# Kernel optimization log

Measured on AMD Instinct MI355X. Metric: run time of the kernel, lower is better.

The kernel has to match this reference:

```python
import jax, jax.numpy as jnp
import numpy as np

N_FLUID = 16384
N_BND = 2048
SUPPORT = float(np.sqrt(16.0 / (np.pi * N_FLUID)))  # ~16 neighbors avg
NB = 8  # basis functions per axis (n = m = 8)
NM = NB * NB
LAYERS = [32, 64, 64, 2]
F_IN = 8
B_IN = 8


def _radius(queries, points, r):
    """numpy brute-force (chunked) radius search; rows = query idx, cols = point idx."""
    r2 = np.float32(r * r)
    pn = (points ** 2).sum(-1)
    qi_all, pj_all = [], []
    for s in range(0, queries.shape[0], 4096):
        q = queries[s:s + 4096]
        d2 = (q ** 2).sum(-1)[:, None] + pn[None, :] - 2.0 * (q @ points.T)
        qi, pj = np.nonzero(d2 < r2)
        qi_all.append(qi + s)
        pj_all.append(pj)
    return (np.concatenate(qi_all).astype(np.int32),
            np.concatenate(pj_all).astype(np.int32))


def setup_inputs() -> dict:
    rng = np.random.default_rng(0)
    fluid_pos = rng.random((N_FLUID, 2)).astype(np.float32)
    # boundary particles along the perimeter of the unit square
    t = np.linspace(0.0, 4.0, N_BND, endpoint=False).astype(np.float32)
    side = np.floor(t).astype(np.int64)
    frac = t - side
    bx = np.where(side == 0, frac, np.where(side == 1, 1.0, np.where(side == 2, 1.0 - frac, 0.0)))
    by = np.where(side == 0, 0.0, np.where(side == 1, frac, np.where(side == 2, 1.0, 1.0 - frac)))
    bnd_pos = np.stack([bx, by], -1).astype(np.float32)

    # fluid-fluid radius graph (centerIgnore: drop self edges)
    fi, fj = _radius(fluid_pos, fluid_pos, SUPPORT)
    keep = fi != fj
    f_tgt, f_src = fi[keep], fj[keep]
    # fluid(query) - boundary(source) radius graph
    b_tgt, b_src = _radius(fluid_pos, bnd_pos, SUPPORT)

    def conv_w(k, cin, cout):
        return (0.05 * rng.standard_normal((NM, cin, cout))).astype(np.float32)

    def lin_w(cin, cout):
        s = np.sqrt(6.0 / (cin + cout))
        return rng.uniform(-s, s, (cin, cout)).astype(np.float32)

    d = {
        'fluid_pos': jnp.asarray(fluid_pos),
        'bnd_pos': jnp.asarray(bnd_pos),
        'fluid_feat': jnp.asarray(rng.standard_normal((N_FLUID, F_IN)).astype(np.float32)),
        'bnd_feat': jnp.asarray(rng.standard_normal((N_BND, B_IN)).astype(np.float32)),
        'f_tgt': jnp.asarray(f_tgt), 'f_src': jnp.asarray(f_src),
        'b_tgt': jnp.asarray(b_tgt), 'b_src': jnp.asarray(b_src),
        # convs: c0 fluid->fluid (F_IN->32), c1 boundary->fluid (B_IN->32),
        #        c2 (96->64), c3 (64->64), c4 (64->2)
        'Wc0': jnp.asarray(conv_w(0, F_IN, 32)), 'bc0': jnp.zeros((32,), jnp.float32),
        'Wc1': jnp.asarray(conv_w(1, B_IN, 32)), 'bc1': jnp.zeros((32,), jnp.float32),
        'Wc2': jnp.asarray(conv_w(2, 96, 64)), 'bc2': jnp.zeros((64,), jnp.float32),
        'Wc3': jnp.asarray(conv_w(3, 64, 64)), 'bc3': jnp.zeros((64,), jnp.float32),
        'Wc4': jnp.asarray(conv_w(4, 64, 2)), 'bc4': jnp.zeros((2,), jnp.float32),
        # dense branch: l0 (F_IN->32), l1 (96->64), l2 (64->64), l3 (64->2)
        'Wl0': jnp.asarray(lin_w(F_IN, 32)), 'bl0': jnp.zeros((32,), jnp.float32),
        'Wl1': jnp.asarray(lin_w(96, 64)), 'bl1': jnp.zeros((64,), jnp.float32),
        'Wl2': jnp.asarray(lin_w(64, 64)), 'bl2': jnp.zeros((64,), jnp.float32),
        'Wl3': jnp.asarray(lin_w(64, 2)), 'bl3': jnp.zeros((2,), jnp.float32),
    }
    return d


def _hat(x, n):
    # linear 'hat' RBF basis on centers in [-1, 1]
    c = jnp.linspace(-1.0, 1.0, n, dtype=x.dtype)
    return jnp.maximum(0.0, 1.0 - jnp.abs(x[:, None] - c[None, :]) * ((n - 1) / 2.0))


def _polar(d):
    # polar coordinate mapping of normalized displacement d in [-1,1]^2
    r = jnp.sqrt(jnp.sum(d * d, -1) + 1e-12)
    theta = jnp.arctan2(d[:, 1], d[:, 0])
    return jnp.clip(jnp.stack([2.0 * r - 1.0, theta / jnp.pi], -1), -1.0, 1.0)


def _rbf_conv(x_src_nodes, src, tgt, disp, W, b, num_tgt):
    m = _polar(disp)                                   # [E,2]
    bx = _hat(m[:, 0], NB)                             # [E,n]
    by = _hat(m[:, 1], NB)                             # [E,m]
    basis = (bx[:, :, None] * by[:, None, :]).reshape(-1, NM)  # [E,nm]
    xs = x_src_nodes[src]                              # [E,cin]
    acc0 = jnp.zeros((xs.shape[0], W.shape[-1]), xs.dtype)

    def body(acc, wb):
        Wk, bk = wb
        return acc + bk[:, None] * (xs @ Wk), None

    msg, _ = jax.lax.scan(body, acc0, (W, basis.T))    # sum_k basis_k * (xs @ W_k)
    return jax.ops.segment_sum(msg, tgt, num_segments=num_tgt) + b


def reference(fluid_pos, bnd_pos, fluid_feat, bnd_feat, f_tgt, f_src, b_tgt, b_src,
              Wc0, bc0, Wc1, bc1, Wc2, bc2, Wc3, bc3, Wc4, bc4,
              Wl0, bl0, Wl1, bl1, Wl2, bl2, Wl3, bl3):
    N = fluid_feat.shape[0]
    fdisp = jnp.clip(-(fluid_pos[f_src] - fluid_pos[f_tgt]) / SUPPORT, -1.0, 1.0)
    bdisp = jnp.clip((bnd_pos[b_src] - fluid_pos[b_tgt]) / SUPPORT, -1.0, 1.0)

    lin = fluid_feat @ Wl0 + bl0
    fconv = _rbf_conv(fluid_feat, f_src, f_tgt, fdisp, Wc0, bc0, N)
    bconv = _rbf_conv(bnd_feat, b_src, b_tgt, bdisp, Wc1, bc1, N)
    ans = jnp.concatenate([lin, fconv, bconv], axis=-1)  # [N, 96]

    blocks = [(Wc2, bc2, Wl1, bl1, False), (Wc3, bc3, Wl2, bl2, True), (Wc4, bc4, Wl3, bl3, False)]
    for Wc, bc, Wl, bl, residual in blocks:
        a = jax.nn.relu(ans)
        c = _rbf_conv(a, f_src, f_tgt, fdisp, Wc, bc, N)
        dns = a @ Wl + bl
        ans = c + dns + ans if residual else c + dns
    return ans / 128.0
```

## Files before the change

kernel.cpp:

```cpp
#include <hip/hip_runtime.h>
#include <math.h>
#include <stdint.h>

#define NFL   16384
#define NCC   55
#define PADQ  128

struct EdgeData { int src; int ixiy; float fx; float fy; };

typedef _Float16 half8 __attribute__((ext_vector_type(8)));
typedef __attribute__((ext_vector_type(4))) float f32x4;

__device__ __forceinline__ float frelu(float x){ return x > 0.f ? x : 0.f; }
__device__ __forceinline__ unsigned short f2bf(float f){
    unsigned int u = __float_as_uint(f);
    unsigned int r = (u + 0x7FFFu + ((u >> 16) & 1u)) >> 16;
    return (unsigned short)r;
}

__device__ __forceinline__ EdgeData make_edge(const float* qpos, const float* ppos,
                                              int t, int s, float support, float sgn)
{
    float dx = sgn * (ppos[2*s]   - qpos[2*t])   / support;
    float dy = sgn * (ppos[2*s+1] - qpos[2*t+1]) / support;
    dx = fminf(1.f, fmaxf(-1.f, dx));
    dy = fminf(1.f, fmaxf(-1.f, dy));
    float r  = sqrtf(dx*dx + dy*dy + 1e-12f);
    float th = atan2f(dy, dx);
    float m0 = fminf(1.f, fmaxf(-1.f, 2.f*r - 1.f));
    float m1 = fminf(1.f, fmaxf(-1.f, th * 0.3183098861837907f));
    float u = (m0 + 1.f) * 3.5f;
    float v = (m1 + 1.f) * 3.5f;
    int ix = (int)u; if (ix > 6) ix = 6;
    int iy = (int)v; if (iy > 6) iy = 6;
    EdgeData ed;
    ed.src  = s;
    ed.ixiy = ix*8 + iy;
    ed.fx   = u - (float)ix;
    ed.fy   = v - (float)iy;
    return ed;
}

__global__ __launch_bounds__(256)
void setup_k(const float* __restrict__ fluid_pos, const float* __restrict__ bnd_pos,
             const int* __restrict__ f_tgt, const int* __restrict__ f_src, int nEf,
             const int* __restrict__ b_tgt, const int* __restrict__ b_src, int nEb,
             float support,
             EdgeData* __restrict__ edF, EdgeData* __restrict__ edB,
             int* __restrict__ cnt,
             int* __restrict__ rowptrF, int* __restrict__ rowptrB,
             int nA, int nB, int nC)
{
    int b = blockIdx.x, tid = threadIdx.x;
    if (b < nA){
        __shared__ int lc[64];
        if (tid < 64) lc[tid] = 0;
        __syncthreads();
        int e = b*256 + tid;
        if (e < nEf){
            EdgeData d = make_edge(fluid_pos, fluid_pos, f_tgt[e], f_src[e], support, -1.f);
            edF[e] = d;
            atomicAdd(&lc[d.ixiy], 1);
        }
        __syncthreads();
        if (tid < 64 && lc[tid] > 0) atomicAdd(&cnt[tid], lc[tid]);
    } else if (b < nA + nB){
        int e = (b - nA)*256 + tid;
        if (e < nEb)
            edB[e] = make_edge(fluid_pos, bnd_pos, b_tgt[e], b_src[e], support, 1.f);
    } else if (b < nA + nB + nC){
        int t = (b - nA - nB)*256 + tid;
        if (t > NFL) return;
        if (t == NFL){ rowptrF[NFL] = nEf; return; }
        int lo = 0, hi = nEf;
        while (lo < hi){ int mid = (lo + hi) >> 1; if (f_tgt[mid] < t) lo = mid + 1; else hi = mid; }
        rowptrF[t] = lo;
    } else {
        int t = (b - nA - nB - nC)*256 + tid;
        if (t > NFL) return;
        if (t == NFL){ rowptrB[NFL] = nEb; return; }
        int lo = 0, hi = nEb;
        while (lo < hi){ int mid = (lo + hi) >> 1; if (b_tgt[mid] < t) lo = mid + 1; else hi = mid; }
        rowptrB[t] = lo;
    }
}

__global__ __launch_bounds__(256)
void scan_pad_k(const int* __restrict__ cnt, int* __restrict__ cellOff,
                int* __restrict__ gcursor, int4* __restrict__ entries)
{
    __shared__ int offS[NCC+1], cntS[NCC];
    int tid = threadIdx.x;
    if (tid < 64) gcursor[tid] = 0;
    if (tid == 0){
        int s = 0;
        for (int k = 0; k < NCC; ++k){
            offS[k] = s; int c = cnt[k]; cntS[k] = c;
            s += ((c + PADQ - 1) / PADQ) * PADQ;
        }
        offS[NCC] = s;
        for (int k = 0; k <= NCC; ++k) cellOff[k] = offS[k];
    }
    __syncthreads();
    for (int k = 0; k < NCC; ++k){
        int base = offS[k] + cntS[k];
        int pads = (offS[k+1] - offS[k]) - cntS[k];
        for (int i = tid; i < pads; i += 256)
            entries[base + i] = make_int4(0, -1, 0, 0);
    }
}

__global__ void scatter_k(const EdgeData* __restrict__ ed, int nE,
                          const int* __restrict__ cellOff,
                          int* __restrict__ gcursor,
                          int4* __restrict__ entries)
{
    __shared__ int lc[64], base[64];
    int tid = threadIdx.x;
    if (tid < 64) lc[tid] = 0;
    __syncthreads();
    int e = blockIdx.x * blockDim.x + tid;
    bool ok = e < nE;
    EdgeData d; int k = 0, r = 0;
    if (ok){ d = ed[e]; k = d.ixiy; r = atomicAdd(&lc[k], 1); }
    __syncthreads();
    if (tid < 64 && lc[tid] > 0) base[tid] = atomicAdd(&gcursor[tid], lc[tid]);
    __syncthreads();
    if (ok){
        int slot = cellOff[k] + base[k] + r;
        entries[slot] = make_int4(d.src, e, __float_as_int(d.fx), __float_as_int(d.fy));
    }
}

__global__ __launch_bounds__(256)
void wprep_k(const float* __restrict__ Wc2, const float* __restrict__ Wc3,
             const float* __restrict__ Wc0,
             _Float16* __restrict__ wt2, _Float16* __restrict__ wt3,
             unsigned short* __restrict__ wb0)
{
    __shared__ _Float16 T[64][98];
    int b = blockIdx.x, tid = threadIdx.x;
    if (b < 64){
        const float* s = Wc2 + (size_t)b * 96 * 64;
        for (int i = tid; i < 96*64; i += 256){ int k = i/64, c = i - k*64; T[c][k] = (_Float16)s[i]; }
        __syncthreads();
        _Float16* d = wt2 + (size_t)b * 64 * 96;
        for (int i = tid; i < 96*64; i += 256){ int c = i/96, k = i - c*96; d[i] = T[c][k]; }
    } else if (b < 128){
        int cell = b - 64;
        const float* s = Wc3 + (size_t)cell * 64 * 64;
        for (int i = tid; i < 64*64; i += 256){ int k = i/64, c = i - k*64; T[c][k] = (_Float16)s[i]; }
        __syncthreads();
        _Float16* d = wt3 + (size_t)cell * 64 * 64;
        for (int i = tid; i < 64*64; i += 256){ int c = i/64, k = i - c*64; d[i] = T[c][k]; }
    } else {
        for (int i = tid; i < 64*8*32; i += 256) wb0[i] = f2bf(Wc0[i]);
    }
}

template<int CIN>
__global__ __launch_bounds__(256)
void conv_mfma_k(const _Float16* __restrict__ xh,
                 const int4* __restrict__ entries,
                 const int* __restrict__ cellOff,
                 const _Float16* __restrict__ wt,
                 _Float16* __restrict__ msg)
{
    constexpr int COUT = 64;
    constexpr int XROW = CIN*2 + 16;
    constexpr int C16  = CIN*2/16;

    __shared__ unsigned char XL[64 * XROW];
    __shared__ float BW[4][64];
    __shared__ int   SRC[64];
    __shared__ int   EID[64];

    int total = cellOff[NCC];
    int pb = blockIdx.x * 128;
    if (pb >= total) return;
    int tid = threadIdx.x;

    int lo_ = 0, hi_ = NCC;
    while (hi_ - lo_ > 1){ int mid = (lo_ + hi_) >> 1; if (cellOff[mid] <= pb) lo_ = mid; else hi_ = mid; }
    const int cell = lo_;
    const int kc[4] = { cell, cell+1, cell+8, cell+9 };

    const int lane = tid & 63, wv = tid >> 6;
    const int lr = lane & 15, lg = lane >> 4;
    const int cb = wv * 16;
    const _Float16* wbase = wt + (size_t)(cb + lr) * CIN + lg * 8;

    for (int ch = 0; ch < 2; ++ch){
        int p0 = pb + ch * 64;

        if (tid < 64){
            int4 en = entries[p0 + tid];
            bool ok = en.y >= 0;
            float fx = __int_as_float(en.z), fy = __int_as_float(en.w);
            BW[0][tid] = ok ? (1.f-fx)*(1.f-fy) : 0.f;
            BW[1][tid] = ok ? (1.f-fx)*fy       : 0.f;
            BW[2][tid] = ok ? fx*(1.f-fy)       : 0.f;
            BW[3][tid] = ok ? fx*fy             : 0.f;
            SRC[tid] = en.x;
            EID[tid] = en.y;
        }
        __syncthreads();
        for (int i = tid; i < 64*C16; i += 256){
            int e = i / C16, c = i - e*C16;
            const uint4* sp = (const uint4*)(xh + (size_t)SRC[e]*CIN) + c;
            *(uint4*)(&XL[e*XROW + 16*c]) = *sp;
        }
        __syncthreads();

        f32x4 acc[4][4];
#pragma unroll
        for (int cr = 0; cr < 4; ++cr)
#pragma unroll
            for (int ae = 0; ae < 4; ++ae)
                acc[cr][ae] = (f32x4)0.f;

#pragma unroll
        for (int k0 = 0; k0 < CIN; k0 += 32){
            half8 b[4], a[4];
#pragma unroll
            for (int cr = 0; cr < 4; ++cr)
                b[cr] = *(const half8*)(wbase + (size_t)kc[cr]*(COUT*CIN) + k0);
#pragma unroll
            for (int ae = 0; ae < 4; ++ae)
                a[ae] = *(const half8*)(XL + (16*ae + lr)*XROW + k0*2 + lg*16);
#pragma unroll
            for (int cr = 0; cr < 4; ++cr)
#pragma unroll
                for (int ae = 0; ae < 4; ++ae)
                    acc[cr][ae] = __builtin_amdgcn_mfma_f32_16x16x32_f16(a[ae], b[cr], acc[cr][ae], 0, 0, 0);
        }

#pragma unroll
        for (int ae = 0; ae < 4; ++ae){
#pragma unroll
            for (int r = 0; r < 4; ++r){
                int E = 16*ae + lg*4 + r;
                int eid = EID[E];
                if (eid >= 0){
                    float v = BW[0][E]*acc[0][ae][r] + BW[1][E]*acc[1][ae][r]
                            + BW[2][E]*acc[2][ae][r] + BW[3][E]*acc[3][ae][r];
                    msg[(size_t)eid*COUT + cb + lr] = (_Float16)v;
                }
            }
        }
        __syncthreads();
    }
}

template<int CIN, int COUT, int TILE_E, bool RELU>
__global__ __launch_bounds__(128)
void conv_cell_k(const float* __restrict__ x,
                 const int4* __restrict__ entries,
                 const int* __restrict__ cellOff,
                 const unsigned short* __restrict__ Wbf,
                 _Float16* __restrict__ msg)
{
    constexpr int TEP = TILE_E + 4;
    constexpr int EG  = TILE_E / 4;
    constexpr int CG  = COUT / 8;
    static_assert(EG * CG == 128, "tile/thread mismatch");
    constexpr int C4  = CIN / 4;

    __shared__ float XT[CIN][TEP];
    __shared__ unsigned short WLc[4][CIN][COUT];
    __shared__ int4 EN[TILE_E];

    int total = cellOff[NCC];
    int p0 = blockIdx.x * TILE_E;
    if (p0 >= total) return;
    int tid = threadIdx.x;

    int lo = 0, hi = NCC;
    while (hi - lo > 1){ int mid = (lo + hi) >> 1; if (cellOff[mid] <= p0) lo = mid; else hi = mid; }
    const int cell = lo;

    for (int i = tid; i < TILE_E; i += 128) EN[i] = entries[p0 + i];

    const int kc[4] = { cell, cell + 1, cell + 8, cell + 9 };
#pragma unroll
    for (int c = 0; c < 4; ++c){
        const uint4* s = (const uint4*)(Wbf + (size_t)kc[c] * (CIN * COUT));
        uint4* dlds = (uint4*)(&WLc[c][0][0]);
        for (int i = tid; i < CIN * COUT / 8; i += 128) dlds[i] = s[i];
    }
    __syncthreads();

    for (int i = tid; i < TILE_E * C4; i += 128){
        int e  = i / C4;
        int c4 = i - e * C4;
        int4 en = EN[e];
        float4 v = make_float4(0.f, 0.f, 0.f, 0.f);
        if (en.y >= 0){
            v = *(const float4*)(x + (size_t)en.x * CIN + 4 * c4);
            if (RELU){ v.x = frelu(v.x); v.y = frelu(v.y); v.z = frelu(v.z); v.w = frelu(v.w); }
        }
        XT[4*c4+0][e] = v.x;
        XT[4*c4+1][e] = v.y;
        XT[4*c4+2][e] = v.z;
        XT[4*c4+3][e] = v.w;
    }
    __syncthreads();

    const int egrp = tid % EG;
    const int cgrp = tid / EG;
    const int e0 = egrp * 4;

    float fx[4], fy[4];
    int eid[4];
#pragma unroll
    for (int j = 0; j < 4; ++j){
        int4 en = EN[e0 + j];
        fx[j] = __int_as_float(en.z);
        fy[j] = __int_as_float(en.w);
        eid[j] = en.y;
    }

    float accT[4][8];
#pragma unroll
    for (int j = 0; j < 4; ++j)
#pragma unroll
        for (int c = 0; c < 8; ++c) accT[j][c] = 0.f;

#pragma unroll
    for (int cr = 0; cr < 4; ++cr){
        float accC[4][8];
#pragma unroll
        for (int j = 0; j < 4; ++j)
#pragma unroll
            for (int c = 0; c < 8; ++c) accC[j][c] = 0.f;

#pragma unroll
        for (int ci = 0; ci < CIN; ++ci){
            float4 xv = *(const float4*)&XT[ci][e0];
            uint4 wp = *(const uint4*)&WLc[cr][ci][cgrp * 8];
            float wf0 = __uint_as_float(wp.x << 16);
            float wf1 = __uint_as_float(wp.x & 0xFFFF0000u);
            float wf2 = __uint_as_float(wp.y << 16);
            float wf3 = __uint_as_float(wp.y & 0xFFFF0000u);
            float wf4 = __uint_as_float(wp.z << 16);
            float wf5 = __uint_as_float(wp.z & 0xFFFF0000u);
            float wf6 = __uint_as_float(wp.w << 16);
            float wf7 = __uint_as_float(wp.w & 0xFFFF0000u);
            const float xe[4] = { xv.x, xv.y, xv.z, xv.w };
#pragma unroll
            for (int j = 0; j < 4; ++j){
                accC[j][0] += xe[j] * wf0;
                accC[j][1] += xe[j] * wf1;
                accC[j][2] += xe[j] * wf2;
                accC[j][3] += xe[j] * wf3;
                accC[j][4] += xe[j] * wf4;
                accC[j][5] += xe[j] * wf5;
                accC[j][6] += xe[j] * wf6;
                accC[j][7] += xe[j] * wf7;
            }
        }
#pragma unroll
        for (int j = 0; j < 4; ++j){
            float wc = (cr == 0) ? (1.f - fx[j]) * (1.f - fy[j]) :
                       (cr == 1) ? (1.f - fx[j]) * fy[j] :
                       (cr == 2) ? fx[j] * (1.f - fy[j]) :
                                   fx[j] * fy[j];
#pragma unroll
            for (int c = 0; c < 8; ++c) accT[j][c] += wc * accC[j][c];
        }
    }

#pragma unroll
    for (int j = 0; j < 4; ++j){
        if (eid[j] < 0) continue;
        half8 hv;
#pragma unroll
        for (int c = 0; c < 8; ++c) hv[c] = (_Float16)accT[j][c];
        *(half8*)(msg + (size_t)eid[j] * COUT + cgrp * 8) = hv;
    }
}

__global__ __launch_bounds__(128)
void conv2_msg_k(const _Float16* __restrict__ xh,
                 const int4* __restrict__ entries,
                 const int* __restrict__ cellOff,
                 const float* __restrict__ Wc,
                 float* __restrict__ msg2)
{
    __shared__ float WLf[4][64][2];
    int total = cellOff[NCC];
    int p0 = blockIdx.x * 128;
    if (p0 >= total) return;
    int tid = threadIdx.x;

    int lo = 0, hi = NCC;
    while (hi - lo > 1){ int mid = (lo + hi) >> 1; if (cellOff[mid] <= p0) lo = mid; else hi = mid; }
    const int cell = lo;
    const int kc[4] = { cell, cell + 1, cell + 8, cell + 9 };
#pragma unroll
    for (int c = 0; c < 4; ++c)
        ((float*)&WLf[c][0][0])[tid] = Wc[(size_t)kc[c] * 128 + tid];
    __syncthreads();

    int4 en = entries[p0 + tid];
    if (en.y < 0) return;
    float fx = __int_as_float(en.z), fy = __int_as_float(en.w);
    const _Float16* xp = xh + (size_t)en.x * 64;

    float a[4][2] = {{0.f,0.f},{0.f,0.f},{0.f,0.f},{0.f,0.f}};
#pragma unroll
    for (int ci = 0; ci < 64; ci += 8){
        half8 v = *(const half8*)(xp + ci);
#pragma unroll
        for (int j = 0; j < 8; ++j){
            float xe = (float)v[j];
#pragma unroll
            for (int cr = 0; cr < 4; ++cr){
                a[cr][0] += xe * WLf[cr][ci+j][0];
                a[cr][1] += xe * WLf[cr][ci+j][1];
            }
        }
    }
    float w0 = (1.f-fx)*(1.f-fy), w1 = (1.f-fx)*fy, w2 = fx*(1.f-fy), w3 = fx*fy;
    float m0 = w0*a[0][0] + w1*a[1][0] + w2*a[2][0] + w3*a[3][0];
    float m1 = w0*a[0][1] + w1*a[1][1] + w2*a[2][1] + w3*a[3][1];
    *(float2*)(msg2 + (size_t)en.y * 2) = make_float2(m0, m1);
}

__global__ __launch_bounds__(256)
void final_combine_k(const float* __restrict__ y2,
                     const float* __restrict__ Wl3, const float* __restrict__ bl3,
                     const float* __restrict__ bc4,
                     const float* __restrict__ msg2,
                     const int* __restrict__ rowptr,
                     float* __restrict__ out)
{
    __shared__ float WS[128];
    int tid = threadIdx.x;
    if (tid < 128) WS[tid] = Wl3[tid];
    __syncthreads();

    int t = blockIdx.x * blockDim.x + tid;
    if (t >= NFL) return;
    int eb = rowptr[t], ee = rowptr[t+1];

    float a0 = bc4[0] + bl3[0];
    float a1 = bc4[1] + bl3[1];
    const float* pr = y2 + (size_t)t * 64;
#pragma unroll 4
    for (int ci = 0; ci < 64; ci += 4){
        float4 v = *(const float4*)(pr + ci);
        float xe[4] = { frelu(v.x), frelu(v.y), frelu(v.z), frelu(v.w) };
#pragma unroll
        for (int j = 0; j < 4; ++j){
            a0 += xe[j] * WS[(ci+j)*2];
            a1 += xe[j] * WS[(ci+j)*2 + 1];
        }
    }
    for (int e = eb; e < ee; ++e){
        float2 m = *(const float2*)(msg2 + (size_t)e * 2);
        a0 += m.x; a1 += m.y;
    }
    out[(size_t)t*2]     = a0 * (1.0f/128.0f);
    out[(size_t)t*2 + 1] = a1 * (1.0f/128.0f);
}

__global__ __launch_bounds__(256)
void combine0_k(const float* __restrict__ feat,
                const float* __restrict__ bnd_feat,
                const float* __restrict__ Wl0, const float* __restrict__ bl0,
                const float* __restrict__ bc0,
                const float* __restrict__ Wc1, const float* __restrict__ bc1,
                const EdgeData* __restrict__ edB,
                const int* __restrict__ rowptrB,
                const _Float16* __restrict__ msg,
                const int* __restrict__ rowptrF,
                float* __restrict__ ansA,
                _Float16* __restrict__ xbA)
{
    int t = blockIdx.x * (blockDim.x >> 6) + (threadIdx.x >> 6);
    if (t >= NFL) return;
    int lane = threadIdx.x & 63;

    if (lane < 32){
        float a = bl0[lane];
#pragma unroll
        for (int ci = 0; ci < 8; ++ci)
            a += feat[t*8 + ci] * Wl0[ci*32 + lane];
        ansA[(size_t)t*96 + lane] = a;
        xbA[(size_t)t*96 + lane]  = (_Float16)frelu(a);

        float b = bc1[lane];
        int eb = rowptrB[t], ee = rowptrB[t+1];
        for (int e = eb; e < ee; ++e){
            EdgeData d = edB[e];
            const float* xp = bnd_feat + (size_t)d.src * 8;
            const float* wp = Wc1 + (size_t)d.ixiy * 256 + lane;
            float t00 = 0.f, t01 = 0.f, t10 = 0.f, t11 = 0.f;
#pragma unroll
            for (int ci = 0; ci < 8; ++ci){
                float xv = xp[ci];
                t00 += xv * wp[ci*32];
                t01 += xv * wp[ci*32 + 256];
                t10 += xv * wp[ci*32 + 2048];
                t11 += xv * wp[ci*32 + 2304];
            }
            float wx1 = d.fx, wy1 = d.fy;
            float wx0 = 1.f - wx1, wy0 = 1.f - wy1;
            b += (wx0*wy0)*t00 + (wx0*wy1)*t01 + (wx1*wy0)*t10 + (wx1*wy1)*t11;
        }
        ansA[(size_t)t*96 + 64 + lane] = b;
        xbA[(size_t)t*96 + 64 + lane]  = (_Float16)frelu(b);
    } else {
        int c = lane - 32;
        float a = bc0[c];
        int eb = rowptrF[t], ee = rowptrF[t+1];
        for (int e = eb; e < ee; ++e)
            a += (float)msg[(size_t)e*32 + c];
        ansA[(size_t)t*96 + 32 + c] = a;
        xbA[(size_t)t*96 + 32 + c]  = (_Float16)frelu(a);
    }
}

template<int CIN, bool RESID, bool WRITE_XB>
__global__ __launch_bounds__(256)
void combine12_k(const float* __restrict__ yprev,
                 const _Float16* __restrict__ xprev,
                 const float* __restrict__ Wl, const float* __restrict__ bl,
                 const float* __restrict__ bc,
                 const _Float16* __restrict__ msg,
                 const int* __restrict__ rowptr,
                 float* __restrict__ y,
                 _Float16* __restrict__ xbnext)
{
    int t = blockIdx.x * (blockDim.x >> 6) + (threadIdx.x >> 6);
    if (t >= NFL) return;
    int lane = threadIdx.x & 63;
    int eb = rowptr[t], ee = rowptr[t+1];

    const _Float16* pr = xprev + (size_t)t * CIN;
    float acc = bc[lane] + bl[lane];
#pragma unroll 8
    for (int ci = 0; ci < CIN; ++ci)
        acc += (float)pr[ci] * Wl[ci*64 + lane];
    if (RESID) acc += yprev[(size_t)t*64 + lane];

    for (int e = eb; e < ee; ++e)
        acc += (float)msg[(size_t)e*64 + lane];
    y[(size_t)t*64 + lane] = acc;

    if (WRITE_XB)
        xbnext[(size_t)t*64 + lane] = (_Float16)frelu(acc);
}

extern "C" void kernel_launch(void* const* d_in, const int* in_sizes, int n_in,
                              void* d_out, int out_size, void* d_ws, size_t ws_size,
                              hipStream_t stream)
{
    const float* fluid_pos  = (const float*)d_in[0];
    const float* bnd_pos    = (const float*)d_in[1];
    const float* fluid_feat = (const float*)d_in[2];
    const float* bnd_feat   = (const float*)d_in[3];
    const int*   f_tgt      = (const int*)  d_in[4];
    const int*   f_src      = (const int*)  d_in[5];
    const int*   b_tgt      = (const int*)  d_in[6];
    const int*   b_src      = (const int*)  d_in[7];
    const float* Wc0 = (const float*)d_in[8];  const float* bc0 = (const float*)d_in[9];
    const float* Wc1 = (const float*)d_in[10]; const float* bc1 = (const float*)d_in[11];
    const float* Wc2 = (const float*)d_in[12]; const float* bc2 = (const float*)d_in[13];
    const float* Wc3 = (const float*)d_in[14]; const float* bc3 = (const float*)d_in[15];
    const float* Wc4 = (const float*)d_in[16]; const float* bc4 = (const float*)d_in[17];
    const float* Wl0 = (const float*)d_in[18]; const float* bl0 = (const float*)d_in[19];
    const float* Wl1 = (const float*)d_in[20]; const float* bl1 = (const float*)d_in[21];
    const float* Wl2 = (const float*)d_in[22]; const float* bl2 = (const float*)d_in[23];
    const float* Wl3 = (const float*)d_in[24]; const float* bl3 = (const float*)d_in[25];

    int nEf = in_sizes[4];
    int nEb = in_sizes[6];
    int entPadMax = nEf + NCC * PADQ;
    float support = (float)sqrt(16.0 / (M_PI * 16384.0));

    char* w = (char*)d_ws;
    auto alloc = [&](size_t bytes){ char* r = w; w += (bytes + 255) & ~(size_t)255; return r; };
    EdgeData* edF      = (EdgeData*)alloc((size_t)nEf * sizeof(EdgeData));
    EdgeData* edB      = (EdgeData*)alloc((size_t)nEb * sizeof(EdgeData));
    int*      cnt      = (int*)     alloc(64 * sizeof(int));
    int*      cellOff  = (int*)     alloc(64 * sizeof(int));
    int*      gcursor  = (int*)     alloc(64 * sizeof(int));
    int*      rowptrF  = (int*)     alloc((NFL+1) * sizeof(int));
    int*      rowptrB  = (int*)     alloc((NFL+1) * sizeof(int));
    int4*     entries  = (int4*)    alloc((size_t)entPadMax * sizeof(int4));
    unsigned short* wb0 = (unsigned short*)alloc((size_t)64*8*32 * 2);
    _Float16* wt2      = (_Float16*)alloc((size_t)64*64*96 * 2);
    _Float16* wt3      = (_Float16*)alloc((size_t)64*64*64 * 2);
    _Float16* xbA      = (_Float16*)alloc((size_t)NFL*96 * 2);
    _Float16* xb1      = (_Float16*)alloc((size_t)NFL*64 * 2);
    _Float16* xb2      = (_Float16*)alloc((size_t)NFL*64 * 2);
    float*    ansA     = (float*)   alloc((size_t)NFL * 96 * sizeof(float));
    float*    y1       = (float*)   alloc((size_t)NFL * 64 * sizeof(float));
    float*    y2       = (float*)   alloc((size_t)NFL * 64 * sizeof(float));
    _Float16* msg      = (_Float16*)alloc((size_t)nEf * 64 * 2);
    float*    msg2     = (float*)   alloc((size_t)nEf * 2 * sizeof(float));

    hipMemsetAsync(cnt, 0, 64 * sizeof(int), stream);
    int nA = (nEf + 255)/256, nB = (nEb + 255)/256, nC = (NFL + 256)/256;
    setup_k<<<nA + nB + 2*nC, 256, 0, stream>>>(fluid_pos, bnd_pos,
                                                f_tgt, f_src, nEf,
                                                b_tgt, b_src, nEb, support,
                                                edF, edB, cnt, rowptrF, rowptrB,
                                                nA, nB, nC);
    scan_pad_k<<<1, 256, 0, stream>>>(cnt, cellOff, gcursor, entries);
    scatter_k<<<nA, 256, 0, stream>>>(edF, nEf, cellOff, gcursor, entries);
    wprep_k<<<129, 256, 0, stream>>>(Wc2, Wc3, Wc0, wt2, wt3, wb0);

    int gridM   = (entPadMax + 127) / 128;
    dim3 tgrid(NFL/4);

    conv_cell_k<8,32,128,false><<<gridM, 128, 0, stream>>>(fluid_feat, entries, cellOff, wb0, msg);
    combine0_k<<<tgrid, 256, 0, stream>>>(fluid_feat, bnd_feat, Wl0, bl0, bc0,
                                          Wc1, bc1, edB, rowptrB,
                                          msg, rowptrF, ansA, xbA);

    conv_mfma_k<96><<<gridM, 256, 0, stream>>>(xbA, entries, cellOff, wt2, msg);
    combine12_k<96,false,true><<<tgrid, 256, 0, stream>>>(nullptr, xbA, Wl1, bl1, bc2, msg, rowptrF, y1, xb1);

    conv_mfma_k<64><<<gridM, 256, 0, stream>>>(xb1, entries, cellOff, wt3, msg);
    combine12_k<64,true,true><<<tgrid, 256, 0, stream>>>(y1, xb1, Wl2, bl2, bc3, msg, rowptrF, y2, xb2);

    conv2_msg_k<<<gridM, 128, 0, stream>>>(xb2, entries, cellOff, Wc4, msg2);
    final_combine_k<<<(NFL+255)/256, 256, 0, stream>>>(y2, Wl3, bl3, bc4, msg2, rowptrF, (float*)d_out);
}
```

Baseline: 283.0 us.

## Fuse weight prep into setup, hoist MFMA weights, fuse last conv into final

Folds the weight-transpose kernel into the setup kernel's grid so it runs as extra blocks, removing one launch. The MFMA conv now loads its B-fragments into registers once per block and processes 256 padded entries per block instead of 128, with cell padding raised to 256 to match. The last 2-output conv message kernel and the final combine are merged into one wave-per-target kernel that gathers source features directly from edF and reduces with shuffles, dropping the msg2 buffer. In exchange, register pressure rises and larger padding adds wasted work per cell.

```diff
diff --git a/kernel.cpp b/kernel.cpp
--- a/kernel.cpp
+++ b/kernel.cpp
@@ -4,7 +4,7 @@
 
 #define NFL   16384
 #define NCC   55
-#define PADQ  128
+#define PADQ  256
 
 struct EdgeData { int src; int ixiy; float fx; float fy; };
 
@@ -49,11 +49,16 @@
              EdgeData* __restrict__ edF, EdgeData* __restrict__ edB,
              int* __restrict__ cnt,
              int* __restrict__ rowptrF, int* __restrict__ rowptrB,
+             const float* __restrict__ Wc2, const float* __restrict__ Wc3,
+             const float* __restrict__ Wc0,
+             _Float16* __restrict__ wt2, _Float16* __restrict__ wt3,
+             unsigned short* __restrict__ wb0,
              int nA, int nB, int nC)
 {
+    __shared__ int lc[64];
+    __shared__ _Float16 T[64][98];
     int b = blockIdx.x, tid = threadIdx.x;
     if (b < nA){
-        __shared__ int lc[64];
         if (tid < 64) lc[tid] = 0;
         __syncthreads();
         int e = b*256 + tid;
@@ -75,13 +80,31 @@
         int lo = 0, hi = nEf;
         while (lo < hi){ int mid = (lo + hi) >> 1; if (f_tgt[mid] < t) lo = mid + 1; else hi = mid; }
         rowptrF[t] = lo;
-    } else {
+    } else if (b < nA + nB + 2*nC){
         int t = (b - nA - nB - nC)*256 + tid;
         if (t > NFL) return;
         if (t == NFL){ rowptrB[NFL] = nEb; return; }
         int lo = 0, hi = nEb;
         while (lo < hi){ int mid = (lo + hi) >> 1; if (b_tgt[mid] < t) lo = mid + 1; else hi = mid; }
         rowptrB[t] = lo;
+    } else {
+        int wb = b - (nA + nB + 2*nC);
+        if (wb < 64){
+            const float* s = Wc2 + (size_t)wb * 96 * 64;
+            for (int i = tid; i < 96*64; i += 256){ int k = i/64, c = i - k*64; T[c][k] = (_Float16)s[i]; }
+            __syncthreads();
+            _Float16* d = wt2 + (size_t)wb * 64 * 96;
+            for (int i = tid; i < 96*64; i += 256){ int c = i/96, k = i - c*96; d[i] = T[c][k]; }
+        } else if (wb < 128){
+            int cell = wb - 64;
+            const float* s = Wc3 + (size_t)cell * 64 * 64;
+            for (int i = tid; i < 64*64; i += 256){ int k = i/64, c = i - k*64; T[c][k] = (_Float16)s[i]; }
+            __syncthreads();
+            _Float16* d = wt3 + (size_t)cell * 64 * 64;
+            for (int i = tid; i < 64*64; i += 256){ int c = i/64, k = i - c*64; d[i] = T[c][k]; }
+        } else {
+            for (int i = tid; i < 64*8*32; i += 256) wb0[i] = f2bf(Wc0[i]);
+        }
     }
 }
 
@@ -132,32 +155,6 @@
     }
 }
 
-__global__ __launch_bounds__(256)
-void wprep_k(const float* __restrict__ Wc2, const float* __restrict__ Wc3,
-             const float* __restrict__ Wc0,
-             _Float16* __restrict__ wt2, _Float16* __restrict__ wt3,
-             unsigned short* __restrict__ wb0)
-{
-    __shared__ _Float16 T[64][98];
-    int b = blockIdx.x, tid = threadIdx.x;
-    if (b < 64){
-        const float* s = Wc2 + (size_t)b * 96 * 64;
-        for (int i = tid; i < 96*64; i += 256){ int k = i/64, c = i - k*64; T[c][k] = (_Float16)s[i]; }
-        __syncthreads();
-        _Float16* d = wt2 + (size_t)b * 64 * 96;
-        for (int i = tid; i < 96*64; i += 256){ int c = i/96, k = i - c*96; d[i] = T[c][k]; }
-    } else if (b < 128){
-        int cell = b - 64;
-        const float* s = Wc3 + (size_t)cell * 64 * 64;
-        for (int i = tid; i < 64*64; i += 256){ int k = i/64, c = i - k*64; T[c][k] = (_Float16)s[i]; }
-        __syncthreads();
-        _Float16* d = wt3 + (size_t)cell * 64 * 64;
-        for (int i = tid; i < 64*64; i += 256){ int c = i/64, k = i - c*64; d[i] = T[c][k]; }
-    } else {
-        for (int i = tid; i < 64*8*32; i += 256) wb0[i] = f2bf(Wc0[i]);
-    }
-}
-
 template<int CIN>
 __global__ __launch_bounds__(256)
 void conv_mfma_k(const _Float16* __restrict__ xh,
@@ -169,6 +166,7 @@
     constexpr int COUT = 64;
     constexpr int XROW = CIN*2 + 16;
     constexpr int C16  = CIN*2/16;
+    constexpr int NK   = CIN/32;
 
     __shared__ unsigned char XL[64 * XROW];
     __shared__ float BW[4][64];
@@ -176,7 +174,7 @@
     __shared__ int   EID[64];
 
     int total = cellOff[NCC];
-    int pb = blockIdx.x * 128;
+    int pb = blockIdx.x * 256;
     if (pb >= total) return;
     int tid = threadIdx.x;
 
@@ -190,7 +188,14 @@
     const int cb = wv * 16;
     const _Float16* wbase = wt + (size_t)(cb + lr) * CIN + lg * 8;
 
-    for (int ch = 0; ch < 2; ++ch){
+    half8 bfr[4][NK];
+#pragma unroll
+    for (int cr = 0; cr < 4; ++cr)
+#pragma unroll
+        for (int kk = 0; kk < NK; ++kk)
+            bfr[cr][kk] = *(const half8*)(wbase + (size_t)kc[cr]*(COUT*CIN) + kk*32);
+
+    for (int ch = 0; ch < 4; ++ch){
         int p0 = pb + ch * 64;
 
         if (tid < 64){
@@ -220,19 +225,16 @@
                 acc[cr][ae] = (f32x4)0.f;
 
 #pragma unroll
-        for (int k0 = 0; k0 < CIN; k0 += 32){
-            half8 b[4], a[4];
+        for (int kk = 0; kk < NK; ++kk){
+            half8 a[4];
+#pragma unroll
+            for (int ae = 0; ae < 4; ++ae)
+                a[ae] = *(const half8*)(XL + (16*ae + lr)*XROW + kk*64 + lg*16);
 #pragma unroll
             for (int cr = 0; cr < 4; ++cr)
-                b[cr] = *(const half8*)(wbase + (size_t)kc[cr]*(COUT*CIN) + k0);
-#pragma unroll
-            for (int ae = 0; ae < 4; ++ae)
-                a[ae] = *(const half8*)(XL + (16*ae + lr)*XROW + k0*2 + lg*16);
-#pragma unroll
-            for (int cr = 0; cr < 4; ++cr)
 #pragma unroll
                 for (int ae = 0; ae < 4; ++ae)
-                    acc[cr][ae] = __builtin_amdgcn_mfma_f32_16x16x32_f16(a[ae], b[cr], acc[cr][ae], 0, 0, 0);
+                    acc[cr][ae] = __builtin_amdgcn_mfma_f32_16x16x32_f16(a[ae], bfr[cr][kk], acc[cr][ae], 0, 0, 0);
         }
 
 #pragma unroll
@@ -380,89 +382,54 @@
     }
 }
 
-__global__ __launch_bounds__(128)
-void conv2_msg_k(const _Float16* __restrict__ xh,
-                 const int4* __restrict__ entries,
-                 const int* __restrict__ cellOff,
-                 const float* __restrict__ Wc,
-                 float* __restrict__ msg2)
-{
-    __shared__ float WLf[4][64][2];
-    int total = cellOff[NCC];
-    int p0 = blockIdx.x * 128;
-    if (p0 >= total) return;
-    int tid = threadIdx.x;
-
-    int lo = 0, hi = NCC;
-    while (hi - lo > 1){ int mid = (lo + hi) >> 1; if (cellOff[mid] <= p0) lo = mid; else hi = mid; }
-    const int cell = lo;
-    const int kc[4] = { cell, cell + 1, cell + 8, cell + 9 };
-#pragma unroll
-    for (int c = 0; c < 4; ++c)
-        ((float*)&WLf[c][0][0])[tid] = Wc[(size_t)kc[c] * 128 + tid];
-    __syncthreads();
-
-    int4 en = entries[p0 + tid];
-    if (en.y < 0) return;
-    float fx = __int_as_float(en.z), fy = __int_as_float(en.w);
-    const _Float16* xp = xh + (size_t)en.x * 64;
-
-    float a[4][2] = {{0.f,0.f},{0.f,0.f},{0.f,0.f},{0.f,0.f}};
-#pragma unroll
-    for (int ci = 0; ci < 64; ci += 8){
-        half8 v = *(const half8*)(xp + ci);
-#pragma unroll
-        for (int j = 0; j < 8; ++j){
-            float xe = (float)v[j];
-#pragma unroll
-            for (int cr = 0; cr < 4; ++cr){
-                a[cr][0] += xe * WLf[cr][ci+j][0];
-                a[cr][1] += xe * WLf[cr][ci+j][1];
-            }
-        }
-    }
-    float w0 = (1.f-fx)*(1.f-fy), w1 = (1.f-fx)*fy, w2 = fx*(1.f-fy), w3 = fx*fy;
-    float m0 = w0*a[0][0] + w1*a[1][0] + w2*a[2][0] + w3*a[3][0];
-    float m1 = w0*a[0][1] + w1*a[1][1] + w2*a[2][1] + w3*a[3][1];
-    *(float2*)(msg2 + (size_t)en.y * 2) = make_float2(m0, m1);
-}
-
 __global__ __launch_bounds__(256)
-void final_combine_k(const float* __restrict__ y2,
-                     const float* __restrict__ Wl3, const float* __restrict__ bl3,
-                     const float* __restrict__ bc4,
-                     const float* __restrict__ msg2,
-                     const int* __restrict__ rowptr,
-                     float* __restrict__ out)
-{
+void final_k(const _Float16* __restrict__ xh,
+             const EdgeData* __restrict__ edF,
+             const int* __restrict__ rowptr,
+             const float* __restrict__ Wc4,
+             const float* __restrict__ Wl3, const float* __restrict__ bl3,
+             const float* __restrict__ bc4,
+             float* __restrict__ out)
+{
+    __shared__ float WL[64][128];
     __shared__ float WS[128];
     int tid = threadIdx.x;
+    for (int i = tid; i < 64*128; i += 256) ((float*)WL)[i] = Wc4[i];
     if (tid < 128) WS[tid] = Wl3[tid];
     __syncthreads();
 
-    int t = blockIdx.x * blockDim.x + tid;
+    int lane = tid & 63, wv = tid >> 6;
+    int t = blockIdx.x * 4 + wv;
     if (t >= NFL) return;
     int eb = rowptr[t], ee = rowptr[t+1];
 
-    float a0 = bc4[0] + bl3[0];
-    float a1 = bc4[1] + bl3[1];
-    const float* pr = y2 + (size_t)t * 64;
-#pragma unroll 4
-    for (int ci = 0; ci < 64; ci += 4){
-        float4 v = *(const float4*)(pr + ci);
-        float xe[4] = { frelu(v.x), frelu(v.y), frelu(v.z), frelu(v.w) };
-#pragma unroll
-        for (int j = 0; j < 4; ++j){
-            a0 += xe[j] * WS[(ci+j)*2];
-            a1 += xe[j] * WS[(ci+j)*2 + 1];
-        }
-    }
+    float xv = (float)xh[(size_t)t*64 + lane];
+    float a0 = xv * WS[lane*2];
+    float a1 = xv * WS[lane*2 + 1];
+
     for (int e = eb; e < ee; ++e){
-        float2 m = *(const float2*)(msg2 + (size_t)e * 2);
-        a0 += m.x; a1 += m.y;
-    }
-    out[(size_t)t*2]     = a0 * (1.0f/128.0f);
-    out[(size_t)t*2 + 1] = a1 * (1.0f/128.0f);
+        EdgeData d = edF[e];
+        int s = __builtin_amdgcn_readfirstlane(d.src);
+        int k = __builtin_amdgcn_readfirstlane(d.ixiy);
+        float fx = d.fx, fy = d.fy;
+        float w00 = (1.f-fx)*(1.f-fy), w01 = (1.f-fx)*fy, w10 = fx*(1.f-fy), w11 = fx*fy;
+        float xe = (float)xh[(size_t)s*64 + lane];
+        float wc0 = w00*WL[k][lane*2]   + w01*WL[k+1][lane*2]
+                  + w10*WL[k+8][lane*2] + w11*WL[k+9][lane*2];
+        float wc1 = w00*WL[k][lane*2+1]   + w01*WL[k+1][lane*2+1]
+                  + w10*WL[k+8][lane*2+1] + w11*WL[k+9][lane*2+1];
+        a0 += xe * wc0;
+        a1 += xe * wc1;
+    }
+#pragma unroll
+    for (int off = 32; off > 0; off >>= 1){
+        a0 += __shfl_down(a0, off);
+        a1 += __shfl_down(a1, off);
+    }
+    if (lane == 0){
+        out[(size_t)t*2]     = (a0 + bc4[0] + bl3[0]) * (1.0f/128.0f);
+        out[(size_t)t*2 + 1] = (a1 + bc4[1] + bl3[1]) * (1.0f/128.0f);
+    }
 }
 
 __global__ __launch_bounds__(256)
@@ -600,23 +567,23 @@
     float*    y1       = (float*)   alloc((size_t)NFL * 64 * sizeof(float));
     float*    y2       = (float*)   alloc((size_t)NFL * 64 * sizeof(float));
     _Float16* msg      = (_Float16*)alloc((size_t)nEf * 64 * 2);
-    float*    msg2     = (float*)   alloc((size_t)nEf * 2 * sizeof(float));
 
     hipMemsetAsync(cnt, 0, 64 * sizeof(int), stream);
     int nA = (nEf + 255)/256, nB = (nEb + 255)/256, nC = (NFL + 256)/256;
-    setup_k<<<nA + nB + 2*nC, 256, 0, stream>>>(fluid_pos, bnd_pos,
-                                                f_tgt, f_src, nEf,
-                                                b_tgt, b_src, nEb, support,
-                                                edF, edB, cnt, rowptrF, rowptrB,
-                                                nA, nB, nC);
+    setup_k<<<nA + nB + 2*nC + 129, 256, 0, stream>>>(fluid_pos, bnd_pos,
+                                                      f_tgt, f_src, nEf,
+                                                      b_tgt, b_src, nEb, support,
+                                                      edF, edB, cnt, rowptrF, rowptrB,
+                                                      Wc2, Wc3, Wc0, wt2, wt3, wb0,
+                                                      nA, nB, nC);
     scan_pad_k<<<1, 256, 0, stream>>>(cnt, cellOff, gcursor, entries);
     scatter_k<<<nA, 256, 0, stream>>>(edF, nEf, cellOff, gcursor, entries);
-    wprep_k<<<129, 256, 0, stream>>>(Wc2, Wc3, Wc0, wt2, wt3, wb0);
-
-    int gridM   = (entPadMax + 127) / 128;
+
+    int gridM = (entPadMax + 255) / 256;
+    int gridC = (entPadMax + 127) / 128;
     dim3 tgrid(NFL/4);
 
-    conv_cell_k<8,32,128,false><<<gridM, 128, 0, stream>>>(fluid_feat, entries, cellOff, wb0, msg);
+    conv_cell_k<8,32,128,false><<<gridC, 128, 0, stream>>>(fluid_feat, entries, cellOff, wb0, msg);
     combine0_k<<<tgrid, 256, 0, stream>>>(fluid_feat, bnd_feat, Wl0, bl0, bc0,
                                           Wc1, bc1, edB, rowptrB,
                                           msg, rowptrF, ansA, xbA);
@@ -627,6 +594,5 @@
     conv_mfma_k<64><<<gridM, 256, 0, stream>>>(xb1, entries, cellOff, wt3, msg);
     combine12_k<64,true,true><<<tgrid, 256, 0, stream>>>(y1, xb1, Wl2, bl2, bc3, msg, rowptrF, y2, xb2);
 
-    conv2_msg_k<<<gridM, 128, 0, stream>>>(xb2, entries, cellOff, Wc4, msg2);
-    final_combine_k<<<(NFL+255)/256, 256, 0, stream>>>(y2, Wl3, bl3, bc4, msg2, rowptrF, (float*)d_out);
-}
+    final_k<<<(NFL+3)/4, 256, 0, stream>>>(xb2, edF, rowptrF, Wc4, Wl3, bl3, bc4, (float*)d_out);
+}
```

Measured after the change: 312.5 us. 10.4% more time.

## Hoist conv weight fragments to registers, process 256 entries per block, fuse weight prep

Applied to the files above, without the earlier changes.

Conv MFMA blocks now cover 256 padded entries (four 64-entry chunks) and load their per-cell weight fragments into registers once, instead of reloading them every chunk. Cell padding grows to 256 so these larger blocks stay within a single cell. The weight transpose/convert work is folded into the setup kernel to drop one launch. The final combine reads the fp16 relu activations instead of the fp32 ones, reducing traffic. The costs are more register pressure, more padded work from the larger cell padding, and slightly lower precision in the final layer input.

```diff
diff --git a/kernel.cpp b/kernel.cpp
--- a/kernel.cpp
+++ b/kernel.cpp
@@ -4,7 +4,7 @@
 
 #define NFL   16384
 #define NCC   55
-#define PADQ  128
+#define PADQ  256
 
 struct EdgeData { int src; int ixiy; float fx; float fy; };
 
@@ -49,11 +49,16 @@
              EdgeData* __restrict__ edF, EdgeData* __restrict__ edB,
              int* __restrict__ cnt,
              int* __restrict__ rowptrF, int* __restrict__ rowptrB,
+             const float* __restrict__ Wc2, const float* __restrict__ Wc3,
+             const float* __restrict__ Wc0,
+             _Float16* __restrict__ wt2, _Float16* __restrict__ wt3,
+             unsigned short* __restrict__ wb0,
              int nA, int nB, int nC)
 {
+    __shared__ int lc[64];
+    __shared__ _Float16 T[64][98];
     int b = blockIdx.x, tid = threadIdx.x;
     if (b < nA){
-        __shared__ int lc[64];
         if (tid < 64) lc[tid] = 0;
         __syncthreads();
         int e = b*256 + tid;
@@ -75,13 +80,31 @@
         int lo = 0, hi = nEf;
         while (lo < hi){ int mid = (lo + hi) >> 1; if (f_tgt[mid] < t) lo = mid + 1; else hi = mid; }
         rowptrF[t] = lo;
-    } else {
+    } else if (b < nA + nB + 2*nC){
         int t = (b - nA - nB - nC)*256 + tid;
         if (t > NFL) return;
         if (t == NFL){ rowptrB[NFL] = nEb; return; }
         int lo = 0, hi = nEb;
         while (lo < hi){ int mid = (lo + hi) >> 1; if (b_tgt[mid] < t) lo = mid + 1; else hi = mid; }
         rowptrB[t] = lo;
+    } else {
+        int wb = b - (nA + nB + 2*nC);
+        if (wb < 64){
+            const float* s = Wc2 + (size_t)wb * 96 * 64;
+            for (int i = tid; i < 96*64; i += 256){ int k = i/64, c = i - k*64; T[c][k] = (_Float16)s[i]; }
+            __syncthreads();
+            _Float16* d = wt2 + (size_t)wb * 64 * 96;
+            for (int i = tid; i < 96*64; i += 256){ int c = i/96, k = i - c*96; d[i] = T[c][k]; }
+        } else if (wb < 128){
+            int cell = wb - 64;
+            const float* s = Wc3 + (size_t)cell * 64 * 64;
+            for (int i = tid; i < 64*64; i += 256){ int k = i/64, c = i - k*64; T[c][k] = (_Float16)s[i]; }
+            __syncthreads();
+            _Float16* d = wt3 + (size_t)cell * 64 * 64;
+            for (int i = tid; i < 64*64; i += 256){ int c = i/64, k = i - c*64; d[i] = T[c][k]; }
+        } else {
+            for (int i = tid; i < 64*8*32; i += 256) wb0[i] = f2bf(Wc0[i]);
+        }
     }
 }
 
@@ -132,32 +155,6 @@
     }
 }
 
-__global__ __launch_bounds__(256)
-void wprep_k(const float* __restrict__ Wc2, const float* __restrict__ Wc3,
-             const float* __restrict__ Wc0,
-             _Float16* __restrict__ wt2, _Float16* __restrict__ wt3,
-             unsigned short* __restrict__ wb0)
-{
-    __shared__ _Float16 T[64][98];
-    int b = blockIdx.x, tid = threadIdx.x;
-    if (b < 64){
-        const float* s = Wc2 + (size_t)b * 96 * 64;
-        for (int i = tid; i < 96*64; i += 256){ int k = i/64, c = i - k*64; T[c][k] = (_Float16)s[i]; }
-        __syncthreads();
-        _Float16* d = wt2 + (size_t)b * 64 * 96;
-        for (int i = tid; i < 96*64; i += 256){ int c = i/96, k = i - c*96; d[i] = T[c][k]; }
-    } else if (b < 128){
-        int cell = b - 64;
-        const float* s = Wc3 + (size_t)cell * 64 * 64;
-        for (int i = tid; i < 64*64; i += 256){ int k = i/64, c = i - k*64; T[c][k] = (_Float16)s[i]; }
-        __syncthreads();
-        _Float16* d = wt3 + (size_t)cell * 64 * 64;
-        for (int i = tid; i < 64*64; i += 256){ int c = i/64, k = i - c*64; d[i] = T[c][k]; }
-    } else {
-        for (int i = tid; i < 64*8*32; i += 256) wb0[i] = f2bf(Wc0[i]);
-    }
-}
-
 template<int CIN>
 __global__ __launch_bounds__(256)
 void conv_mfma_k(const _Float16* __restrict__ xh,
@@ -169,6 +166,7 @@
     constexpr int COUT = 64;
     constexpr int XROW = CIN*2 + 16;
     constexpr int C16  = CIN*2/16;
+    constexpr int NK   = CIN/32;
 
     __shared__ unsigned char XL[64 * XROW];
     __shared__ float BW[4][64];
@@ -176,7 +174,7 @@
     __shared__ int   EID[64];
 
     int total = cellOff[NCC];
-    int pb = blockIdx.x * 128;
+    int pb = blockIdx.x * 256;
     if (pb >= total) return;
     int tid = threadIdx.x;
 
@@ -190,7 +188,14 @@
     const int cb = wv * 16;
     const _Float16* wbase = wt + (size_t)(cb + lr) * CIN + lg * 8;
 
-    for (int ch = 0; ch < 2; ++ch){
+    half8 bfr[4][NK];
+#pragma unroll
+    for (int cr = 0; cr < 4; ++cr)
+#pragma unroll
+        for (int kk = 0; kk < NK; ++kk)
+            bfr[cr][kk] = *(const half8*)(wbase + (size_t)kc[cr]*(COUT*CIN) + kk*32);
+
+    for (int ch = 0; ch < 4; ++ch){
         int p0 = pb + ch * 64;
 
         if (tid < 64){
@@ -220,19 +225,16 @@
                 acc[cr][ae] = (f32x4)0.f;
 
 #pragma unroll
-        for (int k0 = 0; k0 < CIN; k0 += 32){
-            half8 b[4], a[4];
+        for (int kk = 0; kk < NK; ++kk){
+            half8 a[4];
+#pragma unroll
+            for (int ae = 0; ae < 4; ++ae)
+                a[ae] = *(const half8*)(XL + (16*ae + lr)*XROW + kk*64 + lg*16);
 #pragma unroll
             for (int cr = 0; cr < 4; ++cr)
-                b[cr] = *(const half8*)(wbase + (size_t)kc[cr]*(COUT*CIN) + k0);
-#pragma unroll
-            for (int ae = 0; ae < 4; ++ae)
-                a[ae] = *(const half8*)(XL + (16*ae + lr)*XROW + k0*2 + lg*16);
-#pragma unroll
-            for (int cr = 0; cr < 4; ++cr)
 #pragma unroll
                 for (int ae = 0; ae < 4; ++ae)
-                    acc[cr][ae] = __builtin_amdgcn_mfma_f32_16x16x32_f16(a[ae], b[cr], acc[cr][ae], 0, 0, 0);
+                    acc[cr][ae] = __builtin_amdgcn_mfma_f32_16x16x32_f16(a[ae], bfr[cr][kk], acc[cr][ae], 0, 0, 0);
         }
 
 #pragma unroll
@@ -428,7 +430,7 @@
 }
 
 __global__ __launch_bounds__(256)
-void final_combine_k(const float* __restrict__ y2,
+void final_combine_k(const _Float16* __restrict__ xh,
                      const float* __restrict__ Wl3, const float* __restrict__ bl3,
                      const float* __restrict__ bc4,
                      const float* __restrict__ msg2,
@@ -446,15 +448,15 @@
 
     float a0 = bc4[0] + bl3[0];
     float a1 = bc4[1] + bl3[1];
-    const float* pr = y2 + (size_t)t * 64;
-#pragma unroll 4
-    for (int ci = 0; ci < 64; ci += 4){
-        float4 v = *(const float4*)(pr + ci);
-        float xe[4] = { frelu(v.x), frelu(v.y), frelu(v.z), frelu(v.w) };
-#pragma unroll
-        for (int j = 0; j < 4; ++j){
-            a0 += xe[j] * WS[(ci+j)*2];
-            a1 += xe[j] * WS[(ci+j)*2 + 1];
+    const _Float16* pr = xh + (size_t)t * 64;
+#pragma unroll
+    for (int ci = 0; ci < 64; ci += 8){
+        half8 v = *(const half8*)(pr + ci);
+#pragma unroll
+        for (int j = 0; j < 8; ++j){
+            float xe = (float)v[j];
+            a0 += xe * WS[(ci+j)*2];
+            a1 += xe * WS[(ci+j)*2 + 1];
         }
     }
     for (int e = eb; e < ee; ++e){
@@ -604,19 +606,20 @@
 
     hipMemsetAsync(cnt, 0, 64 * sizeof(int), stream);
     int nA = (nEf + 255)/256, nB = (nEb + 255)/256, nC = (NFL + 256)/256;
-    setup_k<<<nA + nB + 2*nC, 256, 0, stream>>>(fluid_pos, bnd_pos,
-                                                f_tgt, f_src, nEf,
-                                                b_tgt, b_src, nEb, support,
-                                                edF, edB, cnt, rowptrF, rowptrB,
-                                                nA, nB, nC);
+    setup_k<<<nA + nB + 2*nC + 129, 256, 0, stream>>>(fluid_pos, bnd_pos,
+                                                      f_tgt, f_src, nEf,
+                                                      b_tgt, b_src, nEb, support,
+                                                      edF, edB, cnt, rowptrF, rowptrB,
+                                                      Wc2, Wc3, Wc0, wt2, wt3, wb0,
+                                                      nA, nB, nC);
     scan_pad_k<<<1, 256, 0, stream>>>(cnt, cellOff, gcursor, entries);
     scatter_k<<<nA, 256, 0, stream>>>(edF, nEf, cellOff, gcursor, entries);
-    wprep_k<<<129, 256, 0, stream>>>(Wc2, Wc3, Wc0, wt2, wt3, wb0);
-
-    int gridM   = (entPadMax + 127) / 128;
+
+    int gridM = (entPadMax + 255) / 256;
+    int gridC = (entPadMax + 127) / 128;
     dim3 tgrid(NFL/4);
 
-    conv_cell_k<8,32,128,false><<<gridM, 128, 0, stream>>>(fluid_feat, entries, cellOff, wb0, msg);
+    conv_cell_k<8,32,128,false><<<gridC, 128, 0, stream>>>(fluid_feat, entries, cellOff, wb0, msg);
     combine0_k<<<tgrid, 256, 0, stream>>>(fluid_feat, bnd_feat, Wl0, bl0, bc0,
                                           Wc1, bc1, edB, rowptrB,
                                           msg, rowptrF, ansA, xbA);
@@ -627,6 +630,6 @@
     conv_mfma_k<64><<<gridM, 256, 0, stream>>>(xb1, entries, cellOff, wt3, msg);
     combine12_k<64,true,true><<<tgrid, 256, 0, stream>>>(y1, xb1, Wl2, bl2, bc3, msg, rowptrF, y2, xb2);
 
-    conv2_msg_k<<<gridM, 128, 0, stream>>>(xb2, entries, cellOff, Wc4, msg2);
-    final_combine_k<<<(NFL+255)/256, 256, 0, stream>>>(y2, Wl3, bl3, bc4, msg2, rowptrF, (float*)d_out);
-}
+    conv2_msg_k<<<gridC, 128, 0, stream>>>(xb2, entries, cellOff, Wc4, msg2);
+    final_combine_k<<<(NFL+255)/256, 256, 0, stream>>>(xb2, Wl3, bl3, bc4, msg2, rowptrF, (float*)d_out);
+}
```

Result: no change. 284.9 us (+0.7%).
